# Kernel tuning notes

Measured on AMD Instinct MI355X. Metric: run time of the kernel, lower is better.

## Reference

```python
import math
import jax, jax.numpy as jnp
import numpy as np

L, H, C, T_MAX, V = 4, 12, 768, 1024, 50257
D = C // H
EPS = 1e-5


def setup_inputs() -> dict:
    key = jax.random.key(0)
    ks = iter(jax.random.split(key, 32))
    s = 0.02
    inp = {
        "idx": jax.random.randint(next(ks), (2, 1024), 0, V, dtype=jnp.int32),
        "wte": jax.random.normal(next(ks), (V, C), jnp.float32) * s,
        "wpe": jax.random.normal(next(ks), (T_MAX, C), jnp.float32) * s,
        # per-layer stacked params, weights stored [in, out]
        "ln1_w": jnp.ones((L, C), jnp.float32),
        "ln1_b": jnp.zeros((L, C), jnp.float32),
        "qkv_w": jax.random.normal(next(ks), (L, C, 3 * C), jnp.float32) * s,
        "qkv_b": jnp.zeros((L, 3 * C), jnp.float32),
        "proj_w": jax.random.normal(next(ks), (L, C, C), jnp.float32) * (s / math.sqrt(2 * L)),
        "proj_b": jnp.zeros((L, C), jnp.float32),
        "ln2_w": jnp.ones((L, C), jnp.float32),
        "ln2_b": jnp.zeros((L, C), jnp.float32),
        "fc_w": jax.random.normal(next(ks), (L, C, 4 * C), jnp.float32) * s,
        "fc_b": jnp.zeros((L, 4 * C), jnp.float32),
        "fc2_w": jax.random.normal(next(ks), (L, 4 * C, C), jnp.float32) * (s / math.sqrt(2 * L)),
        "fc2_b": jnp.zeros((L, C), jnp.float32),
        "lnf_w": jnp.ones((C,), jnp.float32),
        "lnf_b": jnp.zeros((C,), jnp.float32),
        "head_w": jax.random.normal(next(ks), (C, V), jnp.float32) * s,
    }
    return inp


def _layernorm(x, w, b):
    mu = jnp.mean(x, axis=-1, keepdims=True)
    var = jnp.mean(jnp.square(x - mu), axis=-1, keepdims=True)
    return (x - mu) * jax.lax.rsqrt(var + EPS) * w + b


def _new_gelu(x):
    k = math.sqrt(2.0 / math.pi)
    return 0.5 * x * (1.0 + jnp.tanh(k * (x + 0.044715 * x * x * x)))


def _gpt_forward(idx, wte, wpe, layer_params, lnf_w, lnf_b, head_w):
    B, T = idx.shape
    x = wte[idx] + wpe[:T][None, :, :]  # [B, T, C]
    causal = jnp.tril(jnp.ones((T, T), bool))

    def block(x, p):
        ln1w, ln1b, qkvw, qkvb, pw, pb, ln2w, ln2b, fcw, fcb, fc2w, fc2b = p
        h = _layernorm(x, ln1w, ln1b)
        qkv = h @ qkvw + qkvb  # [B, T, 3C]
        q, k, v = jnp.split(qkv, 3, axis=-1)
        # [B, H, T, D]
        q = q.reshape(B, T, H, D).transpose(0, 2, 1, 3)
        k = k.reshape(B, T, H, D).transpose(0, 2, 1, 3)
        v = v.reshape(B, T, H, D).transpose(0, 2, 1, 3)
        att = jnp.einsum("bhtd,bhsd->bhts", q, k) * (1.0 / math.sqrt(D))
        att = jnp.where(causal, att, -jnp.inf)
        att = jax.nn.softmax(att, axis=-1)
        y = jnp.einsum("bhts,bhsd->bhtd", att, v)
        y = y.transpose(0, 2, 1, 3).reshape(B, T, C)
        x = x + (y @ pw + pb)
        h2 = _layernorm(x, ln2w, ln2b)
        m = _new_gelu(h2 @ fcw + fcb) @ fc2w + fc2b
        return x + m, None

    x, _ = jax.lax.scan(block, x, layer_params)
    x = _layernorm(x, lnf_w, lnf_b)
    logits = x @ head_w  # [B, T, V]
    return logits.reshape(B * T, V)


def reference(idx, wte, wpe, ln1_w, ln1_b, qkv_w, qkv_b, proj_w, proj_b,
              ln2_w, ln2_b, fc_w, fc_b, fc2_w, fc2_b, lnf_w, lnf_b, head_w):
    layer_params = (ln1_w, ln1_b, qkv_w, qkv_b, proj_w, proj_b,
                    ln2_w, ln2_b, fc_w, fc_b, fc2_w, fc2_b)
    return _gpt_forward(idx, wte, wpe, layer_params, lnf_w, lnf_b, head_w)
```

## Files before the change

kernel.cpp:

```cpp
#include <hip/hip_runtime.h>
#include <hip/hip_bf16.h>

typedef __hip_bfloat16 bf16;
typedef __attribute__((ext_vector_type(8))) short bf16x8;
typedef __attribute__((ext_vector_type(4))) float f32x4;
typedef __attribute__((ext_vector_type(4), aligned(4))) float f32x4u;

#define NL 4
#define NH 12
#define C 768
#define T 1024
#define NB 2
#define BTOK 2048
#define V 50257
#define DH 64

__device__ __forceinline__ void gload16(const void* g, void* l) {
  __builtin_amdgcn_global_load_lds(
      (const __attribute__((address_space(1))) void*)g,
      (__attribute__((address_space(3))) void*)l, 16, 0, 0);
}

__device__ __forceinline__ float block_sum(float v, float* red) {
#pragma unroll
  for (int off = 32; off; off >>= 1) v += __shfl_down(v, off);
  int lane = threadIdx.x & 63, wid = threadIdx.x >> 6;
  __syncthreads();
  if (lane == 0) red[wid] = v;
  __syncthreads();
  return red[0] + red[1] + red[2] + red[3];
}

__global__ __launch_bounds__(256) void k_embed(const int* __restrict__ idx,
    const float* __restrict__ wte, const float* __restrict__ wpe,
    float* __restrict__ x) {
  long i = (long)blockIdx.x * 256 + threadIdx.x;
  int bt = (int)(i / C), c = (int)(i % C);
  int t = bt & (T - 1);
  x[i] = wte[(long)idx[bt] * C + c] + wpe[(long)t * C + c];
}

__global__ __launch_bounds__(256) void k_transpose_bf16(const float* __restrict__ W,
    bf16* __restrict__ Wt, int K, int N) {
  __shared__ float tile[32][33];
  long zoff = (long)blockIdx.z * K * N;
  W += zoff;
  Wt += zoff;
  int n0 = blockIdx.x * 32, k0 = blockIdx.y * 32;
  int tx = threadIdx.x, ty = threadIdx.y;
#pragma unroll
  for (int i = 0; i < 4; i++) {
    int k = k0 + ty + i * 8, n = n0 + tx;
    if (k < K && n < N) tile[ty + i * 8][tx] = W[(long)k * N + n];
  }
  __syncthreads();
#pragma unroll
  for (int i = 0; i < 4; i++) {
    int n = n0 + ty + i * 8, k = k0 + tx;
    if (n < N && k < K) Wt[(long)n * K + k] = __float2bfloat16(tile[tx][ty + i * 8]);
  }
}

__global__ __launch_bounds__(256) void k_layernorm(const float* __restrict__ x,
    const float* __restrict__ w, const float* __restrict__ b, bf16* __restrict__ out) {
  __shared__ float red[4];
  long row = blockIdx.x;
  const float* xr = x + row * C;
  int t = threadIdx.x;
  float v0 = xr[t], v1 = xr[t + 256], v2 = xr[t + 512];
  float s = block_sum(v0 + v1 + v2, red);
  float mu = s * (1.0f / C);
  float d0 = v0 - mu, d1 = v1 - mu, d2 = v2 - mu;
  float vs = block_sum(d0 * d0 + d1 * d1 + d2 * d2, red);
  float inv = rsqrtf(vs * (1.0f / C) + 1e-5f);
  bf16* orow = out + row * C;
  orow[t]       = __float2bfloat16(d0 * inv * w[t]       + b[t]);
  orow[t + 256] = __float2bfloat16(d1 * inv * w[t + 256] + b[t + 256]);
  orow[t + 512] = __float2bfloat16(d2 * inv * w[t + 512] + b[t + 512]);
}

__global__ __launch_bounds__(256) void k_attn(const bf16* __restrict__ q,
    const bf16* __restrict__ k, const bf16* __restrict__ vt,
    bf16* __restrict__ yb) {
  __shared__ __align__(16) bf16 Pl[4][16][72];
  int pr = blockIdx.x, bh = blockIdx.y;
  int b = bh / NH, h = bh % NH;
  int tid = threadIdx.x, w = tid >> 6, lane = tid & 63;
  int l15 = lane & 15, hi = lane >> 4;
  const bf16* qbase = q + (long)bh * T * DH;
  const bf16* kbase = k + (long)bh * T * DH;
  const bf16* vbase = vt + (long)bh * DH * T;

  int qt = blockIdx.z ? (T / 64 - 1 - pr) : pr;
  int qrow = qt * 64 + w * 16 + l15;
  bf16x8 qf0 = *(const bf16x8*)(qbase + (long)qrow * DH + hi * 8);
  bf16x8 qf1 = *(const bf16x8*)(qbase + (long)qrow * DH + 32 + hi * 8);

  f32x4 accy[4] = {};
  float m_run = -1e30f, l_run = 0.f;

  int nkt = qt + 1;
  for (int kt = 0; kt < nkt; kt++) {
    int kv0 = kt * 64;
    f32x4 accs[4] = {};
#pragma unroll
    for (int kvi = 0; kvi < 4; kvi++) {
      const bf16* kr = kbase + (long)(kv0 + kvi * 16 + l15) * DH + hi * 8;
      bf16x8 kf0 = *(const bf16x8*)kr;
      bf16x8 kf1 = *(const bf16x8*)(kr + 32);
      accs[kvi] = __builtin_amdgcn_mfma_f32_16x16x32_bf16(kf0, qf0, accs[kvi], 0, 0, 0);
      accs[kvi] = __builtin_amdgcn_mfma_f32_16x16x32_bf16(kf1, qf1, accs[kvi], 0, 0, 0);
    }
    bool diag = (kt == qt);
    float p[4][4];
    float tmax = -1e30f;
#pragma unroll
    for (int kvi = 0; kvi < 4; kvi++)
#pragma unroll
      for (int rr = 0; rr < 4; rr++) {
        float s = accs[kvi][rr];
        if (diag && (kvi * 16 + hi * 4 + rr > w * 16 + l15)) s = -1e30f;
        p[kvi][rr] = s;
        tmax = fmaxf(tmax, s);
      }
    tmax = fmaxf(tmax, __shfl_xor(tmax, 16));
    tmax = fmaxf(tmax, __shfl_xor(tmax, 32));
    float m_new = fmaxf(m_run, tmax);
    float scl = __expf(m_run - m_new);
    float psum = 0.f;
#pragma unroll
    for (int kvi = 0; kvi < 4; kvi++)
#pragma unroll
      for (int rr = 0; rr < 4; rr++) {
        float e = __expf(p[kvi][rr] - m_new);
        p[kvi][rr] = e;
        psum += e;
      }
    psum += __shfl_xor(psum, 16);
    psum += __shfl_xor(psum, 32);
    l_run = l_run * scl + psum;
    m_run = m_new;
#pragma unroll
    for (int rr = 0; rr < 4; rr++) {
      float sy = __shfl(scl, hi * 4 + rr);
#pragma unroll
      for (int j = 0; j < 4; j++) accy[j][rr] *= sy;
    }
#pragma unroll
    for (int kvi = 0; kvi < 4; kvi++) {
      union { bf16 hh[2]; unsigned u; } pk0, pk1;
      pk0.hh[0] = __float2bfloat16(p[kvi][0]);
      pk0.hh[1] = __float2bfloat16(p[kvi][1]);
      pk1.hh[0] = __float2bfloat16(p[kvi][2]);
      pk1.hh[1] = __float2bfloat16(p[kvi][3]);
      *(unsigned*)&Pl[w][l15][kvi * 16 + hi * 4]     = pk0.u;
      *(unsigned*)&Pl[w][l15][kvi * 16 + hi * 4 + 2] = pk1.u;
    }
#pragma unroll
    for (int c = 0; c < 2; c++) {
      bf16x8 pf = *(const bf16x8*)&Pl[w][l15][c * 32 + hi * 8];
#pragma unroll
      for (int j = 0; j < 4; j++) {
        const bf16* vr = vbase + (long)(j * 16 + l15) * T + kv0 + c * 32 + hi * 8;
        bf16x8 vf = *(const bf16x8*)vr;
        accy[j] = __builtin_amdgcn_mfma_f32_16x16x32_bf16(pf, vf, accy[j], 0, 0, 0);
      }
    }
  }
  float inv = 1.0f / l_run;
#pragma unroll
  for (int rr = 0; rr < 4; rr++) {
    float li = __shfl(inv, hi * 4 + rr);
    int qg = qt * 64 + w * 16 + hi * 4 + rr;
#pragma unroll
    for (int j = 0; j < 4; j++)
      yb[((long)(b * T + qg)) * C + h * DH + j * 16 + l15] =
          __float2bfloat16(accy[j][rr] * li);
  }
}

__global__ __launch_bounds__(512, 1) void k_head(const bf16* __restrict__ A,
    const bf16* __restrict__ B, float* __restrict__ Cv) {
  __shared__ __align__(16) char lds[131072];
  int hw = blockIdx.y * 8 + blockIdx.x;
  int L = (hw & 7) * 197 + (hw >> 3);
  int mt = L & 7, nt = L >> 3;
  int m0 = mt * 256, n0 = nt * 256;
  int tid = threadIdx.x, lane = tid & 63, wid = tid >> 6;
  int wm = wid >> 2, wn = wid & 3;
  int l15 = lane & 15, hi = lane >> 4, l7 = lane & 7;
  int sg = (lane & 7) ^ (lane >> 3);
  int srA = wid * 8 + (lane >> 3);
  const bf16* Ab = A + (long)(m0 + srA) * 768 + sg * 8;
  const bf16* Bb = B + (long)(n0 + srA) * 768 + sg * 8;
  auto STAGE = [&](int tile, int h) {
    char* dst = lds + (tile & 1) * 65536 + h * 16384 + wid * 1024;
    const bf16* src = (h < 2 ? Ab : Bb) + (long)((h & 1) * 128) * 768 + tile * 64;
    gload16(src, dst);
    gload16(src + 64 * 768, dst + 8192);
  };
  f32x4 acc[8][4] = {};
  STAGE(0, 0); STAGE(0, 1); STAGE(0, 2); STAGE(0, 3); STAGE(1, 0);
  asm volatile("s_waitcnt vmcnt(2)" ::: "memory");
  __builtin_amdgcn_s_barrier();
  int bro = (wn & 1) * 64;
  int g0 = (hi ^ l7) * 16, g1 = ((4 + hi) ^ l7) * 16;
  for (int t = 0; t < 12; t++) {
    char* ha = lds + (t & 1) * 65536 + wm * 16384;
    char* hb = lds + (t & 1) * 65536 + 32768 + (wn >> 1) * 16384;
    bf16x8 af[4], bv[4];
#pragma unroll
    for (int mf = 0; mf < 4; mf++)
      af[mf] = *(const bf16x8*)(ha + (mf * 16 + l15) * 128 + g0);
#pragma unroll
    for (int nf = 0; nf < 4; nf++)
      bv[nf] = *(const bf16x8*)(hb + (bro + nf * 16 + l15) * 128 + g0);
    if (t + 1 < 12) { STAGE(t + 1, 1); STAGE(t + 1, 2); }
    __builtin_amdgcn_s_barrier();
    __builtin_amdgcn_s_setprio(1);
#pragma unroll
    for (int mf = 0; mf < 4; mf++)
#pragma unroll
      for (int nf = 0; nf < 4; nf++)
        acc[mf][nf] = __builtin_amdgcn_mfma_f32_16x16x32_bf16(af[mf], bv[nf], acc[mf][nf], 0, 0, 0);
    __builtin_amdgcn_s_setprio(0);
    __builtin_amdgcn_s_barrier();
#pragma unroll
    for (int mf = 0; mf < 4; mf++)
      af[mf] = *(const bf16x8*)(ha + ((mf + 4) * 16 + l15) * 128 + g0);
    if (t + 1 < 12) STAGE(t + 1, 3);
    __builtin_amdgcn_s_barrier();
    __builtin_amdgcn_s_setprio(1);
#pragma unroll
    for (int mf = 0; mf < 4; mf++)
#pragma unroll
      for (int nf = 0; nf < 4; nf++)
        acc[mf + 4][nf] = __builtin_amdgcn_mfma_f32_16x16x32_bf16(af[mf], bv[nf], acc[mf + 4][nf], 0, 0, 0);
    __builtin_amdgcn_s_setprio(0);
    __builtin_amdgcn_s_barrier();
#pragma unroll
    for (int mf = 0; mf < 4; mf++)
      af[mf] = *(const bf16x8*)(ha + (mf * 16 + l15) * 128 + g1);
#pragma unroll
    for (int nf = 0; nf < 4; nf++)
      bv[nf] = *(const bf16x8*)(hb + (bro + nf * 16 + l15) * 128 + g1);
    __builtin_amdgcn_s_barrier();
    __builtin_amdgcn_s_setprio(1);
#pragma unroll
    for (int mf = 0; mf < 4; mf++)
#pragma unroll
      for (int nf = 0; nf < 4; nf++)
        acc[mf][nf] = __builtin_amdgcn_mfma_f32_16x16x32_bf16(af[mf], bv[nf], acc[mf][nf], 0, 0, 0);
    __builtin_amdgcn_s_setprio(0);
    __builtin_amdgcn_s_barrier();
#pragma unroll
    for (int mf = 0; mf < 4; mf++)
      af[mf] = *(const bf16x8*)(ha + ((mf + 4) * 16 + l15) * 128 + g1);
    if (t + 2 < 12) STAGE(t + 2, 0);
    __builtin_amdgcn_s_barrier();
    __builtin_amdgcn_s_setprio(1);
#pragma unroll
    for (int mf = 0; mf < 4; mf++)
#pragma unroll
      for (int nf = 0; nf < 4; nf++)
        acc[mf + 4][nf] = __builtin_amdgcn_mfma_f32_16x16x32_bf16(af[mf], bv[nf], acc[mf + 4][nf], 0, 0, 0);
    __builtin_amdgcn_s_setprio(0);
    if (t < 11) {
      if (t + 2 < 12) asm volatile("s_waitcnt vmcnt(2)" ::: "memory");
      else            asm volatile("s_waitcnt vmcnt(0)" ::: "memory");
      __builtin_amdgcn_s_barrier();
    }
  }
  __syncthreads();
  float* Cst = (float*)lds;
#pragma unroll
  for (int rnd = 0; rnd < 4; rnd++) {
#pragma unroll
    for (int mfl = 0; mfl < 2; mfl++) {
      int mf = rnd * 2 + mfl;
#pragma unroll
      for (int nf = 0; nf < 4; nf++)
#pragma unroll
        for (int rr = 0; rr < 4; rr++)
          Cst[(wm * 32 + mfl * 16 + hi * 4 + rr) * 260 + wn * 64 + nf * 16 + l15] =
              acc[mf][nf][rr];
    }
    __syncthreads();
#pragma unroll
    for (int s = 0; s < 8; s++) {
      int gid = tid + s * 512;
      int r = gid >> 6, g = gid & 63;
      int grow = m0 + (r >> 5) * 128 + (rnd * 2 + ((r >> 4) & 1)) * 16 + (r & 15);
      int gcol = n0 + g * 4;
      f32x4 vv = *(const f32x4*)&Cst[r * 260 + g * 4];
      float* dst = Cv + (long)grow * V + gcol;
      if (gcol + 3 < V) {
        *(f32x4u*)dst = vv;
      } else {
#pragma unroll
        for (int e = 0; e < 4; e++)
          if (gcol + e < V) dst[e] = vv[e];
      }
    }
    __syncthreads();
  }
}

#define SBK 64
template <int EPI>
__global__ __launch_bounds__(256) void k_gemm_s(const bf16* __restrict__ A,
    const bf16* __restrict__ B, const float* __restrict__ bias,
    void* __restrict__ Cv, int M, int N, int K, int lda, int ldb, int ldc,
    void* __restrict__ Cv2, void* __restrict__ Cv3) {
  __shared__ __align__(16) bf16 As[2][64][SBK];
  __shared__ __align__(16) bf16 Bs[2][128][SBK];
  int nwg = gridDim.x * gridDim.y;
  int hw = blockIdx.y * gridDim.x + blockIdx.x;
  int logical = (hw & 7) * (nwg >> 3) + (hw >> 3);
  int bx = logical % gridDim.x, by = logical / gridDim.x;
  int m0 = bx * 64, n0 = by * 128;
  int tid = threadIdx.x;
  int lane = tid & 63, w = tid >> 6;
  int l15 = lane & 15, hi = lane >> 4, l7 = lane & 7;
  int srow = lane >> 3;
  int sgr = lane & 7;
  int scol = ((sgr ^ srow) << 3);
  f32x4 acc[4][2] = {};
  const bf16* Ag = A + (long)(m0 + w * 8 + srow) * lda + scol;
  const bf16* Bg = B + (long)(n0 + w * 8 + srow) * ldb + scol;
  int NT = K / SBK;
  auto STAGE = [&](int t) {
    int k0 = t * SBK, b = t & 1;
    gload16(Ag + k0,            &As[b][w * 8][0]);
    gload16(Ag + k0 + 32 * lda, &As[b][w * 8 + 32][0]);
    gload16(Bg + k0,            &Bs[b][w * 8][0]);
    gload16(Bg + k0 + 32 * ldb, &Bs[b][w * 8 + 32][0]);
    gload16(Bg + k0 + 64 * ldb, &Bs[b][w * 8 + 64][0]);
    gload16(Bg + k0 + 96 * ldb, &Bs[b][w * 8 + 96][0]);
  };
  STAGE(0);
  STAGE(1);
  int c0 = (hi ^ l7) << 3, c1 = ((4 + hi) ^ l7) << 3;
  for (int t = 0; t < NT; t++) {
    int b = t & 1;
    if (t + 1 < NT) asm volatile("s_waitcnt vmcnt(6)" ::: "memory");
    else            asm volatile("s_waitcnt vmcnt(0)" ::: "memory");
    __builtin_amdgcn_s_barrier();
    bf16x8 a0[4], a1[4], b0[2], b1[2];
#pragma unroll
    for (int i = 0; i < 4; i++) {
      a0[i] = *(const bf16x8*)&As[b][i * 16 + l15][c0];
      a1[i] = *(const bf16x8*)&As[b][i * 16 + l15][c1];
    }
#pragma unroll
    for (int j = 0; j < 2; j++) {
      b0[j] = *(const bf16x8*)&Bs[b][w * 32 + j * 16 + l15][c0];
      b1[j] = *(const bf16x8*)&Bs[b][w * 32 + j * 16 + l15][c1];
    }
    asm volatile("s_waitcnt lgkmcnt(0)" ::: "memory");
    __builtin_amdgcn_s_barrier();
    if (t + 2 < NT) STAGE(t + 2);
    __builtin_amdgcn_s_setprio(1);
#pragma unroll
    for (int i = 0; i < 4; i++)
#pragma unroll
      for (int j = 0; j < 2; j++) {
        acc[i][j] = __builtin_amdgcn_mfma_f32_16x16x32_bf16(a0[i], b0[j], acc[i][j], 0, 0, 0);
        acc[i][j] = __builtin_amdgcn_mfma_f32_16x16x32_bf16(a1[i], b1[j], acc[i][j], 0, 0, 0);
      }
    __builtin_amdgcn_s_setprio(0);
  }
#pragma unroll
  for (int j = 0; j < 2; j++) {
    int gn = n0 + w * 32 + j * 16 + l15;
    float bv = bias[gn];
#pragma unroll
    for (int i = 0; i < 4; i++)
#pragma unroll
      for (int rr = 0; rr < 4; rr++) {
        int gm = m0 + i * 16 + hi * 4 + rr;
        float v = acc[i][j][rr] + bv;
        if constexpr (EPI == 3) {
          long off = (long)gm * ldc + gn;
          ((float*)Cv)[off] = v + ((float*)Cv)[off];
        } else if constexpr (EPI == 2) {
          float u = 0.7978845608028654f * (v + 0.044715f * v * v * v);
          u = fminf(fmaxf(u, -15.f), 15.f);
          float e2 = __expf(2.f * u);
          float th = (e2 - 1.f) / (e2 + 1.f);
          ((bf16*)Cv)[(long)gm * ldc + gn] = __float2bfloat16(0.5f * v * (1.f + th));
        } else if constexpr (EPI == 5) {
          int gb = gm >> 10, gt = gm & 1023;
          int which = gn / C;
          int r = gn - which * C;
          int h = r >> 6, d = r & 63;
          long bh = (long)(gb * NH + h);
          if (which == 0)
            ((bf16*)Cv)[(bh * T + gt) * DH + d] = __float2bfloat16(v * 0.125f);
          else if (which == 1)
            ((bf16*)Cv2)[(bh * T + gt) * DH + d] = __float2bfloat16(v);
          else
            ((bf16*)Cv3)[(bh * DH + d) * T + gt] = __float2bfloat16(v);
        }
      }
  }
}

extern "C" void kernel_launch(void* const* d_in, const int* in_sizes, int n_in,
                              void* d_out, int out_size, void* d_ws, size_t ws_size,
                              hipStream_t stream) {
  const int*   idx    = (const int*)d_in[0];
  const float* wte    = (const float*)d_in[1];
  const float* wpe    = (const float*)d_in[2];
  const float* ln1_w  = (const float*)d_in[3];
  const float* ln1_b  = (const float*)d_in[4];
  const float* qkv_w  = (const float*)d_in[5];
  const float* qkv_b  = (const float*)d_in[6];
  const float* proj_w = (const float*)d_in[7];
  const float* proj_b = (const float*)d_in[8];
  const float* ln2_w  = (const float*)d_in[9];
  const float* ln2_b  = (const float*)d_in[10];
  const float* fc_w   = (const float*)d_in[11];
  const float* fc_b   = (const float*)d_in[12];
  const float* fc2_w  = (const float*)d_in[13];
  const float* fc2_b  = (const float*)d_in[14];
  const float* lnf_w  = (const float*)d_in[15];
  const float* lnf_b  = (const float*)d_in[16];
  const float* head_w = (const float*)d_in[17];
  (void)in_sizes; (void)n_in; (void)out_size; (void)ws_size;

  char* base = (char*)d_ws;
  size_t off = 0;
  auto alloc = [&](size_t bytes) -> void* {
    void* p = base + off;
    off = (off + bytes + 255) & ~(size_t)255;
    return p;
  };
  bf16* wt_qkv  = (bf16*)alloc((size_t)NL * 3 * C * C * 2);
  bf16* wt_proj = (bf16*)alloc((size_t)NL * C * C * 2);
  bf16* wt_fc   = (bf16*)alloc((size_t)NL * 4 * C * C * 2);
  bf16* wt_fc2  = (bf16*)alloc((size_t)NL * 4 * C * C * 2);
  bf16* wt_head = (bf16*)alloc((size_t)V * C * 2);
  float* x      = (float*)alloc((size_t)BTOK * C * 4);
  bf16*  xb     = (bf16*)alloc((size_t)BTOK * C * 2);
  bf16*  qb     = (bf16*)alloc((size_t)NB * NH * T * DH * 2);
  bf16*  kb     = (bf16*)alloc((size_t)NB * NH * T * DH * 2);
  bf16*  vtb    = (bf16*)alloc((size_t)NB * NH * T * DH * 2);
  bf16*  yb     = (bf16*)alloc((size_t)BTOK * C * 2);
  bf16*  mbuf   = (bf16*)alloc((size_t)BTOK * 4 * C * 2);

  dim3 tb(32, 8);
  k_transpose_bf16<<<dim3(72, 24, NL), tb, 0, stream>>>(qkv_w, wt_qkv, C, 3 * C);
  k_transpose_bf16<<<dim3(24, 24, NL), tb, 0, stream>>>(proj_w, wt_proj, C, C);
  k_transpose_bf16<<<dim3(96, 24, NL), tb, 0, stream>>>(fc_w, wt_fc, C, 4 * C);
  k_transpose_bf16<<<dim3(24, 96, NL), tb, 0, stream>>>(fc2_w, wt_fc2, 4 * C, C);
  k_transpose_bf16<<<dim3((V + 31) / 32, 24, 1), tb, 0, stream>>>(head_w, wt_head, C, V);

  k_embed<<<BTOK * C / 256, 256, 0, stream>>>(idx, wte, wpe, x);

  for (int l = 0; l < NL; l++) {
    k_layernorm<<<BTOK, 256, 0, stream>>>(x, ln1_w + l * C, ln1_b + l * C, xb);
    k_gemm_s<5><<<dim3(32, 18), 256, 0, stream>>>(xb, wt_qkv + (long)l * 3 * C * C,
        qkv_b + l * 3 * C, qb, BTOK, 3 * C, C, C, C, 0, kb, vtb);
    k_attn<<<dim3(T / 128, NB * NH, 2), 256, 0, stream>>>(qb, kb, vtb, yb);
    k_gemm_s<3><<<dim3(32, 6), 256, 0, stream>>>(yb, wt_proj + (long)l * C * C,
        proj_b + l * C, x, BTOK, C, C, C, C, C, nullptr, nullptr);
    k_layernorm<<<BTOK, 256, 0, stream>>>(x, ln2_w + l * C, ln2_b + l * C, xb);
    k_gemm_s<2><<<dim3(32, 24), 256, 0, stream>>>(xb, wt_fc + (long)l * 4 * C * C,
        fc_b + l * 4 * C, mbuf, BTOK, 4 * C, C, C, C, 4 * C, nullptr, nullptr);
    k_gemm_s<3><<<dim3(32, 6), 256, 0, stream>>>(mbuf, wt_fc2 + (long)l * 4 * C * C,
        fc2_b + l * C, x, BTOK, C, 4 * C, 4 * C, 4 * C, C, nullptr, nullptr);
  }
  k_layernorm<<<BTOK, 256, 0, stream>>>(x, lnf_w, lnf_b, xb);
  k_head<<<dim3(8, 197), 512, 0, stream>>>(xb, wt_head, (float*)d_out);
}
```

Measured before the change: 1.007 ms.

## Vectorize weight transpose, fuse embedding with first layernorm, lazy softmax rescale

Rewrites the weight transpose-to-bf16 kernel to use 64x64 tiles with float4 loads and 16-byte bf16 stores, cutting per-element memory transactions on the weight conversion that runs every call. Merges the embedding gather with the first layer's layernorm so x is not written and then re-read by a separate kernel. In attention, the running max and the accumulator rescale are only updated when some row's block max exceeds the running max by more than 8, which skips exp and shuffle work in the common case. The cost is exponentials computed against a stale max, which allows values up to e^8 before normalisation and slightly changes rounding.

```diff
diff --git a/kernel.cpp b/kernel.cpp
--- a/kernel.cpp
+++ b/kernel.cpp
@@ -31,33 +31,43 @@
   return red[0] + red[1] + red[2] + red[3];
 }
 
-__global__ __launch_bounds__(256) void k_embed(const int* __restrict__ idx,
-    const float* __restrict__ wte, const float* __restrict__ wpe,
-    float* __restrict__ x) {
-  long i = (long)blockIdx.x * 256 + threadIdx.x;
-  int bt = (int)(i / C), c = (int)(i % C);
-  int t = bt & (T - 1);
-  x[i] = wte[(long)idx[bt] * C + c] + wpe[(long)t * C + c];
-}
-
 __global__ __launch_bounds__(256) void k_transpose_bf16(const float* __restrict__ W,
     bf16* __restrict__ Wt, int K, int N) {
-  __shared__ float tile[32][33];
+  __shared__ float tile[64][69];
   long zoff = (long)blockIdx.z * K * N;
   W += zoff;
   Wt += zoff;
-  int n0 = blockIdx.x * 32, k0 = blockIdx.y * 32;
-  int tx = threadIdx.x, ty = threadIdx.y;
-#pragma unroll
-  for (int i = 0; i < 4; i++) {
-    int k = k0 + ty + i * 8, n = n0 + tx;
-    if (k < K && n < N) tile[ty + i * 8][tx] = W[(long)k * N + n];
+  int k0 = blockIdx.x * 64, n0 = blockIdx.y * 64;
+  int tid = threadIdx.x;
+  int rr = tid >> 4, rc = (tid & 15) * 4;
+#pragma unroll
+  for (int it = 0; it < 4; it++) {
+    int k = it * 16 + rr;
+    int gn = n0 + rc;
+    const float* src = W + (long)(k0 + k) * N + gn;
+    if (gn + 3 < N) {
+      f32x4 v = *(const f32x4u*)src;
+      tile[k][rc] = v[0]; tile[k][rc + 1] = v[1];
+      tile[k][rc + 2] = v[2]; tile[k][rc + 3] = v[3];
+    } else {
+#pragma unroll
+      for (int e = 0; e < 4; e++)
+        tile[k][rc + e] = (gn + e < N) ? src[e] : 0.0f;
+    }
   }
   __syncthreads();
-#pragma unroll
-  for (int i = 0; i < 4; i++) {
-    int n = n0 + ty + i * 8, k = k0 + tx;
-    if (n < N && k < K) Wt[(long)n * K + k] = __float2bfloat16(tile[tx][ty + i * 8]);
+  int wkc = tid & 7;
+#pragma unroll
+  for (int it = 0; it < 2; it++) {
+    int n = it * 32 + (tid >> 3);
+    int gn = n0 + n;
+    if (gn < N) {
+      union { bf16 h[8]; bf16x8 v; } u;
+#pragma unroll
+      for (int j = 0; j < 8; j++)
+        u.h[j] = __float2bfloat16(tile[wkc * 8 + j][n]);
+      *(bf16x8*)&Wt[(long)gn * K + k0 + wkc * 8] = u.v;
+    }
   }
 }
 
@@ -79,6 +89,31 @@
   orow[t + 512] = __float2bfloat16(d2 * inv * w[t + 512] + b[t + 512]);
 }
 
+__global__ __launch_bounds__(256) void k_embed_ln(const int* __restrict__ idx,
+    const float* __restrict__ wte, const float* __restrict__ wpe,
+    const float* __restrict__ w, const float* __restrict__ b,
+    float* __restrict__ x, bf16* __restrict__ out) {
+  __shared__ float red[4];
+  long row = blockIdx.x;
+  int t = threadIdx.x;
+  int tok = idx[row];
+  int pos = (int)(row & (T - 1));
+  const float* we = wte + (long)tok * C;
+  const float* pe = wpe + (long)pos * C;
+  float v0 = we[t] + pe[t], v1 = we[t + 256] + pe[t + 256], v2 = we[t + 512] + pe[t + 512];
+  float* xr = x + row * C;
+  xr[t] = v0; xr[t + 256] = v1; xr[t + 512] = v2;
+  float s = block_sum(v0 + v1 + v2, red);
+  float mu = s * (1.0f / C);
+  float d0 = v0 - mu, d1 = v1 - mu, d2 = v2 - mu;
+  float vs = block_sum(d0 * d0 + d1 * d1 + d2 * d2, red);
+  float inv = rsqrtf(vs * (1.0f / C) + 1e-5f);
+  bf16* orow = out + row * C;
+  orow[t]       = __float2bfloat16(d0 * inv * w[t]       + b[t]);
+  orow[t + 256] = __float2bfloat16(d1 * inv * w[t + 256] + b[t + 256]);
+  orow[t + 512] = __float2bfloat16(d2 * inv * w[t + 512] + b[t + 512]);
+}
+
 __global__ __launch_bounds__(256) void k_attn(const bf16* __restrict__ q,
     const bf16* __restrict__ k, const bf16* __restrict__ vt,
     bf16* __restrict__ yb) {
@@ -125,27 +160,30 @@
       }
     tmax = fmaxf(tmax, __shfl_xor(tmax, 16));
     tmax = fmaxf(tmax, __shfl_xor(tmax, 32));
-    float m_new = fmaxf(m_run, tmax);
-    float scl = __expf(m_run - m_new);
+    if (!__all(tmax - m_run <= 8.0f)) {
+      float m_new = fmaxf(m_run, tmax);
+      float scl = __expf(m_run - m_new);
+      l_run *= scl;
+#pragma unroll
+      for (int rr = 0; rr < 4; rr++) {
+        float sy = __shfl(scl, hi * 4 + rr);
+#pragma unroll
+        for (int j = 0; j < 4; j++) accy[j][rr] *= sy;
+      }
+      m_run = m_new;
+    }
     float psum = 0.f;
 #pragma unroll
     for (int kvi = 0; kvi < 4; kvi++)
 #pragma unroll
       for (int rr = 0; rr < 4; rr++) {
-        float e = __expf(p[kvi][rr] - m_new);
+        float e = __expf(p[kvi][rr] - m_run);
         p[kvi][rr] = e;
         psum += e;
       }
     psum += __shfl_xor(psum, 16);
     psum += __shfl_xor(psum, 32);
-    l_run = l_run * scl + psum;
-    m_run = m_new;
-#pragma unroll
-    for (int rr = 0; rr < 4; rr++) {
-      float sy = __shfl(scl, hi * 4 + rr);
-#pragma unroll
-      for (int j = 0; j < 4; j++) accy[j][rr] *= sy;
-    }
+    l_run += psum;
 #pragma unroll
     for (int kvi = 0; kvi < 4; kvi++) {
       union { bf16 hh[2]; unsigned u; } pk0, pk1;
@@ -449,17 +487,17 @@
   bf16*  yb     = (bf16*)alloc((size_t)BTOK * C * 2);
   bf16*  mbuf   = (bf16*)alloc((size_t)BTOK * 4 * C * 2);
 
-  dim3 tb(32, 8);
-  k_transpose_bf16<<<dim3(72, 24, NL), tb, 0, stream>>>(qkv_w, wt_qkv, C, 3 * C);
-  k_transpose_bf16<<<dim3(24, 24, NL), tb, 0, stream>>>(proj_w, wt_proj, C, C);
-  k_transpose_bf16<<<dim3(96, 24, NL), tb, 0, stream>>>(fc_w, wt_fc, C, 4 * C);
-  k_transpose_bf16<<<dim3(24, 96, NL), tb, 0, stream>>>(fc2_w, wt_fc2, 4 * C, C);
-  k_transpose_bf16<<<dim3((V + 31) / 32, 24, 1), tb, 0, stream>>>(head_w, wt_head, C, V);
-
-  k_embed<<<BTOK * C / 256, 256, 0, stream>>>(idx, wte, wpe, x);
+  k_transpose_bf16<<<dim3(12, 36, NL), 256, 0, stream>>>(qkv_w, wt_qkv, C, 3 * C);
+  k_transpose_bf16<<<dim3(12, 12, NL), 256, 0, stream>>>(proj_w, wt_proj, C, C);
+  k_transpose_bf16<<<dim3(12, 48, NL), 256, 0, stream>>>(fc_w, wt_fc, C, 4 * C);
+  k_transpose_bf16<<<dim3(48, 12, NL), 256, 0, stream>>>(fc2_w, wt_fc2, 4 * C, C);
+  k_transpose_bf16<<<dim3(12, (V + 63) / 64, 1), 256, 0, stream>>>(head_w, wt_head, C, V);
+
+  k_embed_ln<<<BTOK, 256, 0, stream>>>(idx, wte, wpe, ln1_w, ln1_b, x, xb);
 
   for (int l = 0; l < NL; l++) {
-    k_layernorm<<<BTOK, 256, 0, stream>>>(x, ln1_w + l * C, ln1_b + l * C, xb);
+    if (l > 0)
+      k_layernorm<<<BTOK, 256, 0, stream>>>(x, ln1_w + l * C, ln1_b + l * C, xb);
     k_gemm_s<5><<<dim3(32, 18), 256, 0, stream>>>(xb, wt_qkv + (long)l * 3 * C * C,
         qkv_b + l * 3 * C, qb, BTOK, 3 * C, C, C, C, 0, kb, vtb);
     k_attn<<<dim3(T / 128, NB * NH, 2), 256, 0, stream>>>(qb, kb, vtb, yb);
```

Result: faster. 986.0 us (-2.1%).
